# Kernel optimization log

Hardware: AMD Instinct MI355X
Metric: run time of the kernel (lower is better)

## Reference

```python
import jax, jax.numpy as jnp
import numpy as np

N_HEADS = 16
ROPE_BASE = 10000.0

def rotate_half(x):
    x1, x2 = jnp.split(x, 2, axis=-1)
    return jnp.concatenate([-x2, x1], axis=-1)

def rope_tables(T, D, dtype):
    inv_freq = 1.0 / (ROPE_BASE ** (np.arange(0, D, 2, dtype=np.float32) / D))
    t = np.arange(T, dtype=np.float32)
    freqs = np.outer(t, inv_freq)            # [T, D/2]
    emb = np.concatenate([freqs, freqs], -1)  # [T, D]
    return jnp.asarray(np.cos(emb), dtype), jnp.asarray(np.sin(emb), dtype)

def setup_inputs() -> dict:
    key = jax.random.key(0)
    ks = jax.random.split(key, 5)
    B, T, C, D = 2, 2048, 1024, 64
    s = 0.02
    return {
        "x":  jax.random.normal(ks[0], (B, T, C), jnp.float32),
        "Wq": jax.random.normal(ks[1], (C, C), jnp.float32) * s,
        "Wk": jax.random.normal(ks[2], (C, D), jnp.float32) * s,
        "Wv": jax.random.normal(ks[3], (C, D), jnp.float32) * s,
        "Wo": jax.random.normal(ks[4], (C, C), jnp.float32) * s,
    }

def reference(x, Wq, Wk, Wv, Wo):
    B, T, C = x.shape
    H = N_HEADS
    D = C // H
    scale = D ** -0.5
    q = (x @ Wq).reshape(B, T, H, D).transpose(0, 2, 1, 3)  # [B,H,T,D]
    k = x @ Wk                                              # [B,T,D] single KV head
    v = x @ Wv                                              # [B,T,D]
    cos, sin = rope_tables(T, D, x.dtype)                   # [T,D]
    q = q * cos + rotate_half(q) * sin                      # broadcast over B,H
    k = k * cos + rotate_half(k) * sin                      # broadcast over B
    # MQA causal attention: shared K/V head broadcast to all query heads
    scores = jnp.einsum('bhqd,bkd->bhqk', q, k) * scale     # [B,H,T,T]
    causal = jnp.tril(jnp.ones((T, T), bool))
    scores = jnp.where(causal, scores, jnp.finfo(scores.dtype).min)
    attn = jax.nn.softmax(scores, axis=-1)
    out = jnp.einsum('bhqk,bkd->bhqd', attn, v)             # [B,H,T,D]
    out = out.transpose(0, 2, 1, 3).reshape(B, T, C)
    return out @ Wo
```

## Files before the change

### kernel.cpp

```cpp
#include <hip/hip_runtime.h>
#include <hip/hip_bf16.h>

typedef _Float16 f16;
typedef __attribute__((ext_vector_type(8))) _Float16 f16x8;
typedef __attribute__((ext_vector_type(4))) _Float16 f16x4;
typedef __attribute__((ext_vector_type(4))) float f32x4;

#define MFMA16(a, b, c) __builtin_amdgcn_mfma_f32_16x16x32_f16(a, b, c, 0, 0, 0)

__device__ __forceinline__ void gload_lds16(const void* g, void* l)
{
    __builtin_amdgcn_global_load_lds(
        (const __attribute__((address_space(1))) unsigned int*)g,
        (__attribute__((address_space(3))) unsigned int*)l, 16, 0, 0);
}

__global__ __launch_bounds__(256) void cvt_all_kernel(const float* __restrict__ x, const float* __restrict__ Wq,
                                                      const float* __restrict__ Wk, const float* __restrict__ Wv,
                                                      const float* __restrict__ Wo, f16* __restrict__ xb,
                                                      f16* __restrict__ WallT, f16* __restrict__ WoT)
{
    int i = blockIdx.x * 256 + threadIdx.x;
    if (i < 1048576) {
        float4 v = ((const float4*)x)[i];
        f16x4 o;
        o[0] = (f16)v.x; o[1] = (f16)v.y; o[2] = (f16)v.z; o[3] = (f16)v.w;
        *(f16x4*)(xb + 4 * (size_t)i) = o;
        return;
    }
    const float* src;
    f16* dstbase;
    int n4, k4, ldN;
    if (i < 1114112) {
        int j = i - 1048576;
        n4 = (j & 255) * 4; k4 = (j >> 8) * 4;
        src = Wq; ldN = 1024; dstbase = WallT + (size_t)n4 * 1024;
    } else if (i < 1122304) {
        int j = i - 1114112;
        int p4 = (j & 31) * 4; k4 = (j >> 5) * 4;
        if (p4 < 64) {
            n4 = (p4 >= 16 && p4 < 48) ? (p4 ^ 48) : p4;
            src = Wk;
        } else {
            n4 = p4 - 64;
            src = Wv;
        }
        ldN = 64; dstbase = WallT + (size_t)(1024 + p4) * 1024;
    } else {
        int j = i - 1122304;
        n4 = (j & 255) * 4; k4 = (j >> 8) * 4;
        src = Wo; ldN = 1024; dstbase = WoT + (size_t)n4 * 1024;
    }
    float4 v0 = *(const float4*)(src + (size_t)(k4 + 0) * ldN + n4);
    float4 v1 = *(const float4*)(src + (size_t)(k4 + 1) * ldN + n4);
    float4 v2 = *(const float4*)(src + (size_t)(k4 + 2) * ldN + n4);
    float4 v3 = *(const float4*)(src + (size_t)(k4 + 3) * ldN + n4);
    float a0[4] = {v0.x, v0.y, v0.z, v0.w};
    float a1[4] = {v1.x, v1.y, v1.z, v1.w};
    float a2[4] = {v2.x, v2.y, v2.z, v2.w};
    float a3[4] = {v3.x, v3.y, v3.z, v3.w};
#pragma unroll
    for (int jj = 0; jj < 4; ++jj) {
        f16x4 o;
        o[0] = (f16)a0[jj]; o[1] = (f16)a1[jj]; o[2] = (f16)a2[jj]; o[3] = (f16)a3[jj];
        *(f16x4*)(dstbase + (size_t)jj * 1024 + k4) = o;
    }
}

template<int MODE>
__global__ __launch_bounds__(256) void gemm_bt(const f16* __restrict__ A, const f16* __restrict__ Bt,
                                               void* __restrict__ Cv, f16* __restrict__ kout, f16* __restrict__ vout,
                                               int NBX)
{
    __shared__ __align__(16) f16 As[128 * 64];
    __shared__ __align__(16) f16 Bs[64 * 64];
    int id = blockIdx.x;
    int qn = gridDim.x >> 3;
    int lin = (id & 7) * qn + (id >> 3);
    int bx = lin % NBX, by = lin / NBX;
    int tid = threadIdx.x, lane = tid & 63, wid = tid >> 6;
    int wr = wid >> 1, wc = wid & 1;
    int lrow = lane & 15, gq = lane >> 4;
    f32x4 acc[4][2];
#pragma unroll
    for (int fm = 0; fm < 4; ++fm)
#pragma unroll
        for (int fn = 0; fn < 2; ++fn) acc[fm][fn] = (f32x4){0.f, 0.f, 0.f, 0.f};

    for (int kt = 0; kt < 16; ++kt) {
        int k0 = kt * 64;
#pragma unroll
        for (int i = 0; i < 4; ++i) {
            int c = wid * 4 + i;
            int row = c * 8 + (lane >> 3);
            int slot = (lane & 7) ^ (row & 7);
            gload_lds16(A + (size_t)(by * 128 + row) * 1024 + k0 + slot * 8, &As[c * 512 + lane * 8]);
        }
#pragma unroll
        for (int i = 0; i < 2; ++i) {
            int c = wid * 2 + i;
            int row = c * 8 + (lane >> 3);
            int slot = (lane & 7) ^ (row & 7);
            gload_lds16(Bt + (size_t)(bx * 64 + row) * 1024 + k0 + slot * 8, &Bs[c * 512 + lane * 8]);
        }
        __syncthreads();
#pragma unroll
        for (int ks = 0; ks < 2; ++ks) {
            f16x8 af[4], bf[2];
#pragma unroll
            for (int fm = 0; fm < 4; ++fm) {
                int row = wr * 64 + fm * 16 + lrow;
                int slot = (ks * 4 + gq) ^ (row & 7);
                af[fm] = *(const f16x8*)&As[row * 64 + slot * 8];
            }
#pragma unroll
            for (int fn = 0; fn < 2; ++fn) {
                int row = wc * 32 + fn * 16 + lrow;
                int slot = (ks * 4 + gq) ^ (row & 7);
                bf[fn] = *(const f16x8*)&Bs[row * 64 + slot * 8];
            }
#pragma unroll
            for (int fm = 0; fm < 4; ++fm)
#pragma unroll
                for (int fn = 0; fn < 2; ++fn)
                    acc[fm][fn] = MFMA16(af[fm], bf[fn], acc[fm][fn]);
        }
        __syncthreads();
    }
    if constexpr (MODE == 1) {
        float* C = (float*)Cv;
#pragma unroll
        for (int fm = 0; fm < 4; ++fm)
#pragma unroll
            for (int fn = 0; fn < 2; ++fn)
#pragma unroll
                for (int r = 0; r < 4; ++r) {
                    int row = by * 128 + wr * 64 + fm * 16 + gq * 4 + r;
                    int col = bx * 64 + wc * 32 + fn * 16 + lrow;
                    C[(size_t)row * 1024 + col] = acc[fm][fn][r];
                }
    } else {
        if (bx < 16) {
            f16* C = (f16*)Cv;
#pragma unroll
            for (int fm = 0; fm < 4; ++fm)
#pragma unroll
                for (int fn = 0; fn < 2; ++fn)
#pragma unroll
                    for (int r = 0; r < 4; ++r) {
                        int row = by * 128 + wr * 64 + fm * 16 + gq * 4 + r;
                        int col = bx * 64 + wc * 32 + fn * 16 + lrow;
                        C[(size_t)row * 1024 + col] = (f16)acc[fm][fn][r];
                    }
        } else if (bx == 16) {
            const float L2B = 13.287712379549449f / 64.0f;
            int i = wc * 16 + lrow;
            float invf = exp2f(-(float)(2 * i) * L2B);
#pragma unroll
            for (int fm = 0; fm < 4; ++fm)
#pragma unroll
                for (int r = 0; r < 4; ++r) {
                    int row = by * 128 + wr * 64 + fm * 16 + gq * 4 + r;
                    float t = (float)(row & 2047);
                    float ss, cc;
                    sincosf(t * invf, &ss, &cc);
                    float x1 = acc[fm][0][r], x2 = acc[fm][1][r];
                    kout[(size_t)row * 64 + i]      = (f16)(x1 * cc - x2 * ss);
                    kout[(size_t)row * 64 + i + 32] = (f16)(x2 * cc + x1 * ss);
                }
        } else {
#pragma unroll
            for (int fm = 0; fm < 4; ++fm)
#pragma unroll
                for (int fn = 0; fn < 2; ++fn) {
                    int d = wc * 32 + fn * 16 + lrow;
                    int rowbase = by * 128 + wr * 64 + fm * 16 + gq * 4;
                    f16x4 pw;
#pragma unroll
                    for (int r = 0; r < 4; ++r) pw[r] = (f16)acc[fm][fn][r];
                    *(f16x4*)&vout[(size_t)d * 4096 + rowbase] = pw;
                }
        }
    }
}

#define SOFTMAX(S, LL, PSF) do {                                                    \
    float rs = 0.f;                                                                 \
    _Pragma("unroll")                                                               \
    for (int tt = 0; tt < 4; ++tt) {                                                \
        f16x4 pw;                                                                   \
        _Pragma("unroll")                                                           \
        for (int r = 0; r < 4; ++r) {                                               \
            float pp = exp2f(S[tt][r]); S[tt][r] = pp; pw[r] = (f16)pp;             \
        }                                                                           \
        rs += (S[tt][0] + S[tt][1]) + (S[tt][2] + S[tt][3]);                        \
        *(f16x4*)&PSF[lrow * 64 + ((tt * 16 + g * 4) ^ swl)] = pw;                  \
    }                                                                               \
    LL += rs;                                                                       \
} while (0)

__global__ __launch_bounds__(256, 3) void attn_kernel(const f16* __restrict__ q, const f16* __restrict__ k,
                                                      const f16* __restrict__ vt, f16* __restrict__ ao,
                                                      char* __restrict__ partial)
{
    constexpr int T = 2048;
    int c = blockIdx.x, y = blockIdx.y;
    int b = y >> 3, hA = y & 7, hB = hA + 8;
    int qt, ch;
    if (c < 16)      { qt = 16 + c; ch = 0; }
    else if (c < 32) { qt = c;      ch = 1; }
    else             { qt = 47 - c; ch = 0; }
    int nt = qt + 1;
    int nch = (qt >= 16) ? 2 : 1;
    int tbeg = ch * 16;
    int tend = min(nt, tbeg + 16);

    int tid = threadIdx.x, lane = tid & 63, wid = tid >> 6;
    int lrow = lane & 15, g = lane >> 4;
    int qw = qt * 64 + wid * 16;
    int swl = (lrow & 7) << 3;

    __shared__ __align__(16) f16 Ks[2][64 * 64];
    __shared__ __align__(16) f16 Vs[2][64 * 64];
    __shared__ __align__(16) f16 PsM[4][2][16 * 64];

    const f16* qrowA = q + (size_t)(b * T + qw + lrow) * 1024 + hA * 64;
    const f16* qrowB = qrowA + (hB - hA) * 64;
    f16x8 xA0 = *(const f16x8*)&qrowA[g * 8];
    f16x8 xA1 = *(const f16x8*)&qrowA[g * 8 + 32];
    f16x8 xB0 = *(const f16x8*)&qrowB[g * 8];
    f16x8 xB1 = *(const f16x8*)&qrowB[g * 8 + 32];
    f16x8 qfA0, qfA1, qfB0, qfB1;
    {
        const float qsc = 0.125f * 1.4426950408889634f;
        const float L2B = 13.287712379549449f / 64.0f;
        float t_ = (float)(qw + lrow);
#pragma unroll
        for (int j = 0; j < 8; ++j) {
            int i = g * 8 + j;
            float invf = exp2f(-(float)(2 * i) * L2B);
            float ss, cc;
            sincosf(t_ * invf, &ss, &cc);
            float a0 = (float)xA0[j], a1 = (float)xA1[j];
            qfA0[j] = (f16)((a0 * cc - a1 * ss) * qsc);
            qfA1[j] = (f16)((a1 * cc + a0 * ss) * qsc);
            float b0 = (float)xB0[j], b1 = (float)xB1[j];
            qfB0[j] = (f16)((b0 * cc - b1 * ss) * qsc);
            qfB1[j] = (f16)((b1 * cc + b0 * ss) * qsc);
        }
    }

    float lA = 0.f, lB = 0.f;
    f32x4 oA[4], oB[4];
#pragma unroll
    for (int dt = 0; dt < 4; ++dt) { oA[dt] = (f32x4){0.f,0.f,0.f,0.f}; oB[dt] = (f32x4){0.f,0.f,0.f,0.f}; }

    const f16* kbase = k + (size_t)b * T * 64;
    const f16* vtbase = vt + (size_t)b * T;

    int srow_lo = lane >> 3, sslot = lane & 7;
#define STAGE(buf, t) do {                                                                   \
    _Pragma("unroll")                                                                        \
    for (int i_ = 0; i_ < 2; ++i_) {                                                         \
        int c2 = wid * 2 + i_;                                                               \
        int row = c2 * 8 + srow_lo;                                                          \
        int slot = sslot ^ (row & 7);                                                        \
        gload_lds16(kbase + (size_t)((t) * 64 + row) * 64 + slot * 8,                        \
                    &Ks[buf][c2 * 512 + lane * 8]);                                          \
        gload_lds16(vtbase + (size_t)row * 4096 + (t) * 64 + slot * 8,                       \
                    &Vs[buf][c2 * 512 + lane * 8]);                                          \
    }                                                                                        \
} while (0)

    STAGE(0, tbeg);
    __syncthreads();
    int cur = 0;

    for (int t = tbeg; t < tend; ++t) {
        if (t + 1 < tend) STAGE(cur ^ 1, t + 1);
        f16* PsA = &PsM[wid][0][0];
        f16* PsBf = &PsM[wid][1][0];
        const f16* Kc = &Ks[cur][0];
        const f16* Vc = &Vs[cur][0];

        f32x4 sA[4], sB[4];
        __builtin_amdgcn_s_setprio(1);
#pragma unroll
        for (int tt = 0; tt < 4; ++tt) {
            f16x8 kf0 = *(const f16x8*)&Kc[(tt * 16 + lrow) * 64 + ((g * 8) ^ swl)];
            f16x8 kf1 = *(const f16x8*)&Kc[(tt * 16 + lrow) * 64 + ((32 + g * 8) ^ swl)];
            f32x4 z = (f32x4){0.f, 0.f, 0.f, 0.f};
            z = MFMA16(kf0, qfA0, z);
            z = MFMA16(kf1, qfA1, z);
            sA[tt] = z;
            z = (f32x4){0.f, 0.f, 0.f, 0.f};
            z = MFMA16(kf0, qfB0, z);
            z = MFMA16(kf1, qfB1, z);
            sB[tt] = z;
        }
        __builtin_amdgcn_s_setprio(0);
        if (t == nt - 1) {
            int qab = qw + lrow;
            int kb0 = t * 64 + g * 4;
#pragma unroll
            for (int tt = 0; tt < 4; ++tt)
#pragma unroll
                for (int r = 0; r < 4; ++r)
                    if (kb0 + tt * 16 + r > qab) { sA[tt][r] = -1e30f; sB[tt][r] = -1e30f; }
        }
        SOFTMAX(sA, lA, PsA);
        SOFTMAX(sB, lB, PsBf);
        __builtin_amdgcn_s_setprio(1);
#pragma unroll
        for (int chk = 0; chk < 2; ++chk) {
            f16x8 pfA = *(const f16x8*)&PsA[lrow * 64 + ((chk * 32 + g * 8) ^ swl)];
            f16x8 pfB = *(const f16x8*)&PsBf[lrow * 64 + ((chk * 32 + g * 8) ^ swl)];
#pragma unroll
            for (int dt = 0; dt < 4; ++dt) {
                f16x8 vf = *(const f16x8*)&Vc[(dt * 16 + lrow) * 64 + ((chk * 32 + g * 8) ^ swl)];
                oA[dt] = MFMA16(pfA, vf, oA[dt]);
                oB[dt] = MFMA16(pfB, vf, oB[dt]);
            }
        }
        __builtin_amdgcn_s_setprio(0);
        __syncthreads();
        cur ^= 1;
    }
#undef STAGE
    lA += __shfl_xor(lA, 16); lA += __shfl_xor(lA, 32);
    lB += __shfl_xor(lB, 16); lB += __shfl_xor(lB, 32);
    float lvA[4], lvB[4];
#pragma unroll
    for (int rr = 0; rr < 4; ++rr) { lvA[rr] = __shfl(lA, g * 4 + rr); lvB[rr] = __shfl(lB, g * 4 + rr); }

    if (nch == 1) {
#pragma unroll
        for (int rr = 0; rr < 4; ++rr) {
            float invA = 1.f / lvA[rr];
            float invB = 1.f / lvB[rr];
            int qab = qw + g * 4 + rr;
            size_t rowoff = (size_t)(b * T + qab) * 1024;
#pragma unroll
            for (int dt = 0; dt < 4; ++dt) {
                ao[rowoff + hA * 64 + dt * 16 + lrow] = (f16)(oA[dt][rr] * invA);
                ao[rowoff + hB * 64 + dt * 16 + lrow] = (f16)(oB[dt][rr] * invB);
            }
        }
    } else {
        int bhA = b * 16 + hA, bhB = b * 16 + hB;
        char* slotA = partial + ((size_t)(bhA * 16 + (qt - 16)) * 2 + ch) * 8704;
        char* slotB = partial + ((size_t)(bhB * 16 + (qt - 16)) * 2 + ch) * 8704;
        f16* opA = (f16*)slotA; float* lpA = (float*)(slotA + 8192);
        f16* opB = (f16*)slotB; float* lpB = (float*)(slotB + 8192);
#pragma unroll
        for (int rr = 0; rr < 4; ++rr) {
            float invA = 1.f / lvA[rr];
            float invB = 1.f / lvB[rr];
            int row = wid * 16 + g * 4 + rr;
#pragma unroll
            for (int dt = 0; dt < 4; ++dt) {
                opA[row * 64 + dt * 16 + lrow] = (f16)(oA[dt][rr] * invA);
                opB[row * 64 + dt * 16 + lrow] = (f16)(oB[dt][rr] * invB);
            }
        }
        if (g == 0) {
            lpA[wid * 16 + lrow] = lA;
            lpB[wid * 16 + lrow] = lB;
        }
    }
}

__global__ __launch_bounds__(256) void combine_kernel(const char* __restrict__ partial, f16* __restrict__ ao)
{
    constexpr int T = 2048;
    int qt = 16 + blockIdx.x, bh = blockIdx.y;
    int b = bh >> 4, h = bh & 15;
    int tid = threadIdx.x;
    int row = tid >> 2, dp = (tid & 3) * 16;
    const char* s0 = partial + ((size_t)(bh * 16 + (qt - 16)) * 2) * 8704;
    const char* s1 = s0 + 8704;
    const f16* o0 = (const f16*)s0; const float* l0 = (const float*)(s0 + 8192);
    const f16* o1 = (const f16*)s1; const float* l1 = (const float*)(s1 + 8192);
    float l0r = l0[row], l1r = l1[row];
    float inv = 1.f / (l0r + l1r);
    float w0 = l0r * inv, w1 = l1r * inv;
    f16x8 u0 = ((const f16x8*)(o0 + row * 64 + dp))[0];
    f16x8 u1 = ((const f16x8*)(o0 + row * 64 + dp))[1];
    f16x8 v0 = ((const f16x8*)(o1 + row * 64 + dp))[0];
    f16x8 v1 = ((const f16x8*)(o1 + row * 64 + dp))[1];
    f16x8 r0, r1;
#pragma unroll
    for (int j = 0; j < 8; ++j) {
        r0[j] = (f16)((float)u0[j] * w0 + (float)v0[j] * w1);
        r1[j] = (f16)((float)u1[j] * w0 + (float)v1[j] * w1);
    }
    f16* dst = ao + (size_t)(b * T + qt * 64 + row) * 1024 + h * 64 + dp;
    *(f16x8*)dst = r0;
    *(f16x8*)(dst + 8) = r1;
}

extern "C" void kernel_launch(void* const* d_in, const int* in_sizes, int n_in,
                              void* d_out, int out_size, void* d_ws, size_t ws_size,
                              hipStream_t stream)
{
    (void)in_sizes; (void)n_in; (void)out_size; (void)ws_size;
    const float* x  = (const float*)d_in[0];
    const float* Wq = (const float*)d_in[1];
    const float* Wk = (const float*)d_in[2];
    const float* Wv = (const float*)d_in[3];
    const float* Wo = (const float*)d_in[4];
    float* out = (float*)d_out;

    char* w = (char*)d_ws;
    size_t off = 0;
    auto alloc = [&](size_t bytes) -> void* {
        void* p = (void*)(w + off);
        off += (bytes + 255) & ~(size_t)255;
        return p;
    };
    f16* xb    = (f16*)alloc(4194304ull * 2);
    f16* WallT = (f16*)alloc(1179648ull * 2);
    f16* WoT   = (f16*)alloc(1048576ull * 2);
    f16* qg    = (f16*)alloc(4194304ull * 2);
    f16* krp   = (f16*)alloc(262144ull * 2);
    f16* vt    = (f16*)alloc(262144ull * 2);
    f16* ao    = (f16*)alloc(4194304ull * 2);
    char* partial = (char*)xb;

    cvt_all_kernel<<<4640, 256, 0, stream>>>(x, Wq, Wk, Wv, Wo, xb, WallT, WoT);
    gemm_bt<0><<<576, 256, 0, stream>>>(xb, WallT, qg, krp, vt, 18);
    attn_kernel<<<dim3(48, 16), 256, 0, stream>>>(qg, krp, vt, ao, partial);
    combine_kernel<<<dim3(16, 32), 256, 0, stream>>>(partial, ao);
    gemm_bt<1><<<512, 256, 0, stream>>>(ao, WoT, out, nullptr, nullptr, 16);
}
```

Baseline: 93.93 us.

## Split long attention query tiles three ways, share P LDS buffer, raise occupancy

Query tiles 16-31 are now split into three KV chunks instead of two, and the grid is reordered so heads vary fastest and work is better balanced across 1024 blocks. The first chunk writes directly into the output and saves its row sums, and the combine kernel merges three partials in place. The per-wave P staging buffer is halved by running head A's and head B's softmax and PV sequentially through one buffer, which together with launch bounds of 4 is meant to raise occupancy. The cost is more combine traffic, less overlap between the two heads' softmax and PV, and possible register spills.

```diff
diff --git a/kernel.cpp b/kernel.cpp
--- a/kernel.cpp
+++ b/kernel.cpp
@@ -199,21 +199,20 @@
     LL += rs;                                                                       \
 } while (0)
 
-__global__ __launch_bounds__(256, 3) void attn_kernel(const f16* __restrict__ q, const f16* __restrict__ k,
+__global__ __launch_bounds__(256, 4) void attn_kernel(const f16* __restrict__ q, const f16* __restrict__ k,
                                                       const f16* __restrict__ vt, f16* __restrict__ ao,
                                                       char* __restrict__ partial)
 {
     constexpr int T = 2048;
-    int c = blockIdx.x, y = blockIdx.y;
+    int y = blockIdx.x, c = blockIdx.y;
     int b = y >> 3, hA = y & 7, hB = hA + 8;
-    int qt, ch;
-    if (c < 16)      { qt = 16 + c; ch = 0; }
-    else if (c < 32) { qt = c;      ch = 1; }
-    else             { qt = 47 - c; ch = 0; }
+    int s = c >> 4, j = c & 15;
+    int qt, ch, nch;
+    if (s == 0) { qt = j;      ch = 0;     nch = 1; }
+    else        { qt = 31 - j; ch = s - 1; nch = 3; }
     int nt = qt + 1;
-    int nch = (qt >= 16) ? 2 : 1;
-    int tbeg = ch * 16;
-    int tend = min(nt, tbeg + 16);
+    int tbeg = (nch == 1) ? 0 : ch * nt / 3;
+    int tend = (nch == 1) ? nt : (ch + 1) * nt / 3;
 
     int tid = threadIdx.x, lane = tid & 63, wid = tid >> 6;
     int lrow = lane & 15, g = lane >> 4;
@@ -222,7 +221,7 @@
 
     __shared__ __align__(16) f16 Ks[2][64 * 64];
     __shared__ __align__(16) f16 Vs[2][64 * 64];
-    __shared__ __align__(16) f16 PsM[4][2][16 * 64];
+    __shared__ __align__(16) f16 PsM[4][16 * 64];
 
     const f16* qrowA = q + (size_t)(b * T + qw + lrow) * 1024 + hA * 64;
     const f16* qrowB = qrowA + (hB - hA) * 64;
@@ -236,17 +235,17 @@
         const float L2B = 13.287712379549449f / 64.0f;
         float t_ = (float)(qw + lrow);
 #pragma unroll
-        for (int j = 0; j < 8; ++j) {
-            int i = g * 8 + j;
+        for (int jj = 0; jj < 8; ++jj) {
+            int i = g * 8 + jj;
             float invf = exp2f(-(float)(2 * i) * L2B);
             float ss, cc;
             sincosf(t_ * invf, &ss, &cc);
-            float a0 = (float)xA0[j], a1 = (float)xA1[j];
-            qfA0[j] = (f16)((a0 * cc - a1 * ss) * qsc);
-            qfA1[j] = (f16)((a1 * cc + a0 * ss) * qsc);
-            float b0 = (float)xB0[j], b1 = (float)xB1[j];
-            qfB0[j] = (f16)((b0 * cc - b1 * ss) * qsc);
-            qfB1[j] = (f16)((b1 * cc + b0 * ss) * qsc);
+            float a0 = (float)xA0[jj], a1 = (float)xA1[jj];
+            qfA0[jj] = (f16)((a0 * cc - a1 * ss) * qsc);
+            qfA1[jj] = (f16)((a1 * cc + a0 * ss) * qsc);
+            float b0 = (float)xB0[jj], b1 = (float)xB1[jj];
+            qfB0[jj] = (f16)((b0 * cc - b1 * ss) * qsc);
+            qfB1[jj] = (f16)((b1 * cc + b0 * ss) * qsc);
         }
     }
 
@@ -278,8 +277,7 @@
 
     for (int t = tbeg; t < tend; ++t) {
         if (t + 1 < tend) STAGE(cur ^ 1, t + 1);
-        f16* PsA = &PsM[wid][0][0];
-        f16* PsBf = &PsM[wid][1][0];
+        f16* Ps = &PsM[wid][0];
         const f16* Kc = &Ks[cur][0];
         const f16* Vc = &Vs[cur][0];
 
@@ -308,18 +306,27 @@
                 for (int r = 0; r < 4; ++r)
                     if (kb0 + tt * 16 + r > qab) { sA[tt][r] = -1e30f; sB[tt][r] = -1e30f; }
         }
-        SOFTMAX(sA, lA, PsA);
-        SOFTMAX(sB, lB, PsBf);
+        SOFTMAX(sA, lA, Ps);
         __builtin_amdgcn_s_setprio(1);
 #pragma unroll
         for (int chk = 0; chk < 2; ++chk) {
-            f16x8 pfA = *(const f16x8*)&PsA[lrow * 64 + ((chk * 32 + g * 8) ^ swl)];
-            f16x8 pfB = *(const f16x8*)&PsBf[lrow * 64 + ((chk * 32 + g * 8) ^ swl)];
+            f16x8 pf = *(const f16x8*)&Ps[lrow * 64 + ((chk * 32 + g * 8) ^ swl)];
 #pragma unroll
             for (int dt = 0; dt < 4; ++dt) {
                 f16x8 vf = *(const f16x8*)&Vc[(dt * 16 + lrow) * 64 + ((chk * 32 + g * 8) ^ swl)];
-                oA[dt] = MFMA16(pfA, vf, oA[dt]);
-                oB[dt] = MFMA16(pfB, vf, oB[dt]);
+                oA[dt] = MFMA16(pf, vf, oA[dt]);
+            }
+        }
+        __builtin_amdgcn_s_setprio(0);
+        SOFTMAX(sB, lB, Ps);
+        __builtin_amdgcn_s_setprio(1);
+#pragma unroll
+        for (int chk = 0; chk < 2; ++chk) {
+            f16x8 pf = *(const f16x8*)&Ps[lrow * 64 + ((chk * 32 + g * 8) ^ swl)];
+#pragma unroll
+            for (int dt = 0; dt < 4; ++dt) {
+                f16x8 vf = *(const f16x8*)&Vc[(dt * 16 + lrow) * 64 + ((chk * 32 + g * 8) ^ swl)];
+                oB[dt] = MFMA16(pf, vf, oB[dt]);
             }
         }
         __builtin_amdgcn_s_setprio(0);
@@ -333,7 +340,9 @@
 #pragma unroll
     for (int rr = 0; rr < 4; ++rr) { lvA[rr] = __shfl(lA, g * 4 + rr); lvB[rr] = __shfl(lB, g * 4 + rr); }
 
-    if (nch == 1) {
+    float* l0arr = (float*)(partial + 8650752);
+
+    if (nch == 1 || ch == 0) {
 #pragma unroll
         for (int rr = 0; rr < 4; ++rr) {
             float invA = 1.f / lvA[rr];
@@ -346,10 +355,17 @@
                 ao[rowoff + hB * 64 + dt * 16 + lrow] = (f16)(oB[dt][rr] * invB);
             }
         }
+        if (nch == 3 && g == 0) {
+            int qtx = qt - 16;
+            int bhA = b * 16 + hA, bhB = b * 16 + hB;
+            l0arr[(bhA * 16 + qtx) * 64 + wid * 16 + lrow] = lA;
+            l0arr[(bhB * 16 + qtx) * 64 + wid * 16 + lrow] = lB;
+        }
     } else {
+        int qtx = qt - 16;
         int bhA = b * 16 + hA, bhB = b * 16 + hB;
-        char* slotA = partial + ((size_t)(bhA * 16 + (qt - 16)) * 2 + ch) * 8704;
-        char* slotB = partial + ((size_t)(bhB * 16 + (qt - 16)) * 2 + ch) * 8704;
+        char* slotA = partial + ((size_t)(bhA * 16 + qtx) * 2 + (ch - 1)) * 8448;
+        char* slotB = partial + ((size_t)(bhB * 16 + qtx) * 2 + (ch - 1)) * 8448;
         f16* opA = (f16*)slotA; float* lpA = (float*)(slotA + 8192);
         f16* opB = (f16*)slotB; float* lpB = (float*)(slotB + 8192);
 #pragma unroll
@@ -373,30 +389,35 @@
 __global__ __launch_bounds__(256) void combine_kernel(const char* __restrict__ partial, f16* __restrict__ ao)
 {
     constexpr int T = 2048;
-    int qt = 16 + blockIdx.x, bh = blockIdx.y;
+    int qtx = blockIdx.x, qt = 16 + qtx, bh = blockIdx.y;
     int b = bh >> 4, h = bh & 15;
     int tid = threadIdx.x;
     int row = tid >> 2, dp = (tid & 3) * 16;
-    const char* s0 = partial + ((size_t)(bh * 16 + (qt - 16)) * 2) * 8704;
-    const char* s1 = s0 + 8704;
-    const f16* o0 = (const f16*)s0; const float* l0 = (const float*)(s0 + 8192);
-    const f16* o1 = (const f16*)s1; const float* l1 = (const float*)(s1 + 8192);
-    float l0r = l0[row], l1r = l1[row];
-    float inv = 1.f / (l0r + l1r);
-    float w0 = l0r * inv, w1 = l1r * inv;
-    f16x8 u0 = ((const f16x8*)(o0 + row * 64 + dp))[0];
-    f16x8 u1 = ((const f16x8*)(o0 + row * 64 + dp))[1];
-    f16x8 v0 = ((const f16x8*)(o1 + row * 64 + dp))[0];
-    f16x8 v1 = ((const f16x8*)(o1 + row * 64 + dp))[1];
+    const float* l0arr = (const float*)(partial + 8650752);
+    const char* s1 = partial + ((size_t)(bh * 16 + qtx) * 2 + 0) * 8448;
+    const char* s2 = partial + ((size_t)(bh * 16 + qtx) * 2 + 1) * 8448;
+    float l0 = l0arr[(bh * 16 + qtx) * 64 + row];
+    float l1 = ((const float*)(s1 + 8192))[row];
+    float l2 = ((const float*)(s2 + 8192))[row];
+    float inv = 1.f / (l0 + l1 + l2);
+    float w0 = l0 * inv, w1 = l1 * inv, w2 = l2 * inv;
+    f16* aop = ao + (size_t)(b * T + qt * 64 + row) * 1024 + h * 64 + dp;
+    const f16* o1 = (const f16*)s1 + row * 64 + dp;
+    const f16* o2 = (const f16*)s2 + row * 64 + dp;
+    f16x8 u0 = ((const f16x8*)aop)[0];
+    f16x8 u1 = ((const f16x8*)aop)[1];
+    f16x8 v0 = ((const f16x8*)o1)[0];
+    f16x8 v1 = ((const f16x8*)o1)[1];
+    f16x8 x0 = ((const f16x8*)o2)[0];
+    f16x8 x1 = ((const f16x8*)o2)[1];
     f16x8 r0, r1;
 #pragma unroll
-    for (int j = 0; j < 8; ++j) {
-        r0[j] = (f16)((float)u0[j] * w0 + (float)v0[j] * w1);
-        r1[j] = (f16)((float)u1[j] * w0 + (float)v1[j] * w1);
-    }
-    f16* dst = ao + (size_t)(b * T + qt * 64 + row) * 1024 + h * 64 + dp;
-    *(f16x8*)dst = r0;
-    *(f16x8*)(dst + 8) = r1;
+    for (int jj = 0; jj < 8; ++jj) {
+        r0[jj] = (f16)((float)u0[jj] * w0 + (float)v0[jj] * w1 + (float)x0[jj] * w2);
+        r1[jj] = (f16)((float)u1[jj] * w0 + (float)v1[jj] * w1 + (float)x1[jj] * w2);
+    }
+    ((f16x8*)aop)[0] = r0;
+    ((f16x8*)aop)[1] = r1;
 }
 
 extern "C" void kernel_launch(void* const* d_in, const int* in_sizes, int n_in,
@@ -429,7 +450,7 @@
 
     cvt_all_kernel<<<4640, 256, 0, stream>>>(x, Wq, Wk, Wv, Wo, xb, WallT, WoT);
     gemm_bt<0><<<576, 256, 0, stream>>>(xb, WallT, qg, krp, vt, 18);
-    attn_kernel<<<dim3(48, 16), 256, 0, stream>>>(qg, krp, vt, ao, partial);
+    attn_kernel<<<dim3(16, 64), 256, 0, stream>>>(qg, krp, vt, ao, partial);
     combine_kernel<<<dim3(16, 32), 256, 0, stream>>>(partial, ao);
     gemm_bt<1><<<512, 256, 0, stream>>>(ao, WoT, out, nullptr, nullptr, 16);
 }
```

Result: no change. 94.35 us (+0.4%).
